# Performance work log

Hardware: AMD Instinct MI355X
Metric: run time of the kernel (lower is better)

## Reference

```python
import jax, jax.numpy as jnp
import numpy as np

D_MODEL = 1024
N_HEADS = 16
D_K = D_MODEL // N_HEADS


def setup_inputs() -> dict:
    key = jax.random.key(0)
    ks = jax.random.split(key, 9)
    s = 0.02
    return {
        "x": jax.random.normal(ks[0], (4, 2048, D_MODEL), dtype=jnp.float32),
        "WQ_w": jax.random.normal(ks[1], (D_MODEL, D_MODEL), dtype=jnp.float32) * s,
        "WQ_b": jax.random.normal(ks[2], (D_MODEL,), dtype=jnp.float32) * s,
        "WK_w": jax.random.normal(ks[3], (D_MODEL, D_MODEL), dtype=jnp.float32) * s,
        "WK_b": jax.random.normal(ks[4], (D_MODEL,), dtype=jnp.float32) * s,
        "WV_w": jax.random.normal(ks[5], (D_MODEL, D_MODEL), dtype=jnp.float32) * s,
        "WV_b": jax.random.normal(ks[6], (D_MODEL,), dtype=jnp.float32) * s,
        "Wo_w": jax.random.normal(ks[7], (D_MODEL, D_MODEL), dtype=jnp.float32) * s,
        "Wo_b": jax.random.normal(ks[8], (D_MODEL,), dtype=jnp.float32) * s,
    }


def _rope_cache(T, dtype):
    half = D_K // 2
    freq = 1.0 / (10000.0 ** (2.0 * jnp.arange(half, dtype=dtype) / D_K))
    angles = jnp.arange(T, dtype=dtype)[:, None] * freq[None, :]  # [T, half]
    return jnp.cos(angles), jnp.sin(angles)


def _apply_rope(x, cos, sin):
    # x: [B, H, T, d_k]; cos/sin: [T, d_k//2] broadcast over B,H
    half = x.shape[-1] // 2
    x1, x2 = x[..., :half], x[..., half:]
    return jnp.concatenate([x1 * cos - x2 * sin, x1 * sin + x2 * cos], axis=-1)


def reference(x, WQ_w, WQ_b, WK_w, WK_b, WV_w, WV_b, Wo_w, Wo_b):
    B, T, D = x.shape

    def proj(w, b):
        y = jnp.einsum('btd,ed->bte', x, w) + b
        return y.reshape(B, T, N_HEADS, D_K).transpose(0, 2, 1, 3)  # [B,H,T,d_k]

    q = proj(WQ_w, WQ_b)
    k = proj(WK_w, WK_b)
    v = proj(WV_w, WV_b)

    cos, sin = _rope_cache(T, x.dtype)
    q = _apply_rope(q, cos, sin)
    k = _apply_rope(k, cos, sin)

    scores = jnp.einsum('bhqd,bhkd->bhqk', q, k) / jnp.sqrt(jnp.asarray(D_K, x.dtype))
    causal = jnp.tril(jnp.ones((T, T), dtype=bool))
    scores = jnp.where(causal[None, None, :, :], scores, -jnp.inf)
    attn = jax.nn.softmax(scores, axis=-1)
    out = jnp.einsum('bhqk,bhkd->bhqd', attn, v)
    out = out.transpose(0, 2, 1, 3).reshape(B, T, D)
    return jnp.einsum('btd,ed->bte', out, Wo_w) + Wo_b
```

## Files before the change

kernel.cpp:

```cpp
#include <hip/hip_runtime.h>
#include <math.h>

#define DM 1024
#define NH 16
#define DK 64
#define BB 4
#define TT 2048
#define MTOT (BB*TT)

typedef __bf16 bf16x8 __attribute__((ext_vector_type(8)));
typedef short  s16x4  __attribute__((ext_vector_type(4)));
typedef float  f32x4  __attribute__((ext_vector_type(4)));

__device__ __forceinline__ short f2bf_s(float f) {
    __bf16 h = (__bf16)f;
    return __builtin_bit_cast(short, h);
}

__device__ __forceinline__ float exp2_fast(float x) {
    float r;
    asm("v_exp_f32 %0, %1" : "=v"(r) : "v"(x));
    return r;
}

__device__ __forceinline__ void async_copy16(unsigned short* lds, const unsigned short* g) {
    __builtin_amdgcn_global_load_lds(
        (const __attribute__((address_space(1))) unsigned int*)g,
        (__attribute__((address_space(3))) unsigned int*)lds, 16, 0, 0);
}

__global__ __launch_bounds__(256)
void cvt_all_kernel(const float* __restrict__ x,
                    const float* __restrict__ wq, const float* __restrict__ wk,
                    const float* __restrict__ wv, const float* __restrict__ wo,
                    unsigned short* __restrict__ xb,
                    unsigned short* __restrict__ wqb, unsigned short* __restrict__ wkb,
                    unsigned short* __restrict__ wvb, unsigned short* __restrict__ wob)
{
    const int XB = (MTOT * DM) / 1024;
    int bz = blockIdx.x;
    const float* src; unsigned short* dst; int blk;
    if (bz < XB) { src = x; dst = xb; blk = bz; }
    else {
        int t = bz - XB, which = t >> 10;
        blk = t & 1023;
        if (which == 0)      { src = wq; dst = wqb; }
        else if (which == 1) { src = wk; dst = wkb; }
        else if (which == 2) { src = wv; dst = wvb; }
        else                 { src = wo; dst = wob; }
    }
    int i = blk * 256 + threadIdx.x;
    float4 v = ((const float4*)src)[i];
    ushort4 o;
    o.x = (unsigned short)f2bf_s(v.x); o.y = (unsigned short)f2bf_s(v.y);
    o.z = (unsigned short)f2bf_s(v.z); o.w = (unsigned short)f2bf_s(v.w);
    ((ushort4*)dst)[i] = o;
}

template<int MODE>
__global__ __launch_bounds__(256, 3)
void gemm_bf16_kernel(const unsigned short* __restrict__ X,
                      const unsigned short* __restrict__ W0, const float* __restrict__ b0,
                      const unsigned short* __restrict__ W1, const float* __restrict__ b1,
                      const unsigned short* __restrict__ W2, const float* __restrict__ b2,
                      void* __restrict__ Y0, void* __restrict__ Y1, void* __restrict__ Y2)
{
    const unsigned short* W; const float* bias; void* Yv;
    const int z = blockIdx.z;
    if (z == 0)      { W = W0; bias = b0; Yv = Y0; }
    else if (z == 1) { W = W1; bias = b1; Yv = Y1; }
    else             { W = W2; bias = b2; Yv = Y2; }

    __shared__ __align__(16) unsigned short As[128 * 64];
    __shared__ __align__(16) unsigned short Bs[128 * 64];

    const int tid  = threadIdx.x;
    const int w    = tid >> 6, lane = tid & 63;
    const int quad = lane >> 4, lq = lane & 15;
    const int bm = blockIdx.x * 128, bn = blockIdx.y * 128;
    const int wm = (w >> 1) * 64,   wn = (w & 1) * 64;

    const int srow = lane >> 3;
    const int sg   = (lane & 7) ^ srow;
    const int soff = sg * 8;

    f32x4 acc[4][4];
    #pragma unroll
    for (int i = 0; i < 4; ++i)
        #pragma unroll
        for (int j = 0; j < 4; ++j)
            acc[i][j] = {0.f, 0.f, 0.f, 0.f};

    for (int k0 = 0; k0 < DM; k0 += 64) {
        #pragma unroll
        for (int c = 0; c < 4; ++c) {
            int r0 = w * 32 + c * 8;
            async_copy16(&As[r0 * 64], &X[(size_t)(bm + r0 + srow) * DM + k0 + soff]);
            async_copy16(&Bs[r0 * 64], &W[(size_t)(bn + r0 + srow) * DM + k0 + soff]);
        }
        __syncthreads();

        #pragma unroll
        for (int ks = 0; ks < 2; ++ks) {
            const int gsw = ((ks << 2) + quad) ^ (lq & 7);
            bf16x8 af[4], bfr[4];
            #pragma unroll
            for (int i = 0; i < 4; ++i)
                af[i] = *(const bf16x8*)&As[(wm + i*16 + lq) * 64 + gsw * 8];
            #pragma unroll
            for (int j = 0; j < 4; ++j)
                bfr[j] = *(const bf16x8*)&Bs[(wn + j*16 + lq) * 64 + gsw * 8];
            #pragma unroll
            for (int i = 0; i < 4; ++i)
                #pragma unroll
                for (int j = 0; j < 4; ++j)
                    acc[i][j] = __builtin_amdgcn_mfma_f32_16x16x32_bf16(af[i], bfr[j], acc[i][j], 0, 0, 0);
        }
        __syncthreads();
    }

    if (MODE == 0) {
        #pragma unroll
        for (int j = 0; j < 4; ++j) {
            int n = bn + wn + j*16 + lq;
            float bv = bias[n];
            #pragma unroll
            for (int i = 0; i < 4; ++i)
                #pragma unroll
                for (int r = 0; r < 4; ++r) {
                    int m = bm + wm + i*16 + quad*4 + r;
                    ((float*)Yv)[(size_t)m * DM + n] = acc[i][j][r] + bv;
                }
        }
    } else if (z == 2) {
        #pragma unroll
        for (int j = 0; j < 4; ++j) {
            int n = bn + wn + j*16 + lq;
            float bv = bias[n];
            int h = n >> 6, dk = n & 63;
            #pragma unroll
            for (int i = 0; i < 4; ++i) {
                int m0 = bm + wm + i*16 + quad*4;
                int b = m0 >> 11, t0 = m0 & 2047;
                ushort4 o;
                o.x = (unsigned short)f2bf_s(acc[i][j][0] + bv);
                o.y = (unsigned short)f2bf_s(acc[i][j][1] + bv);
                o.z = (unsigned short)f2bf_s(acc[i][j][2] + bv);
                o.w = (unsigned short)f2bf_s(acc[i][j][3] + bv);
                *(ushort4*)&((unsigned short*)Yv)[((size_t)(b * NH + h) * DK + dk) * TT + t0] = o;
            }
        }
    } else {
        const float QSC = (z == 0) ? 0.125f * 1.44269504f : 1.0f;
        const int h = (bn + wn) >> 6;
        const int b = (bm + wm) >> 11;
        const int tb0 = ((bm + wm) & 2047) + quad * 4;
        #pragma unroll
        for (int jp = 0; jp < 2; ++jp) {
            int dk1 = jp * 16 + lq;
            float freq = exp2f(-(float)dk1 * 0.4152410118f);
            float bv1 = bias[bn + wn + dk1];
            float bv2 = bias[bn + wn + dk1 + 32];
            float s1, c1, s16v, c16v, sb, cb;
            __sincosf(freq, &s1, &c1);
            __sincosf(16.0f * freq, &s16v, &c16v);
            __sincosf((float)tb0 * freq, &sb, &cb);
            #pragma unroll
            for (int i = 0; i < 4; ++i) {
                float cr = cb, sr = sb;
                #pragma unroll
                for (int r = 0; r < 4; ++r) {
                    int t = tb0 + i*16 + r;
                    float v1 = acc[i][jp][r]     + bv1;
                    float v2 = acc[i][jp + 2][r] + bv2;
                    float o1 = (v1 * cr - v2 * sr) * QSC;
                    float o2 = (v1 * sr + v2 * cr) * QSC;
                    size_t base = ((size_t)(b * NH + h) * TT + t) << 6;
                    ((__bf16*)Yv)[base + dk1]      = (__bf16)o1;
                    ((__bf16*)Yv)[base + dk1 + 32] = (__bf16)o2;
                    float cn = cr * c1 - sr * s1;
                    sr = cr * s1 + sr * c1;
                    cr = cn;
                }
                float cbn = cb * c16v - sb * s16v;
                sb = cb * s16v + sb * c16v;
                cb = cbn;
            }
        }
    }
}

__global__ __launch_bounds__(256, 3)
void attn_kernel(const unsigned short* __restrict__ Q, const unsigned short* __restrict__ K,
                 const unsigned short* __restrict__ Vt_g, unsigned short* __restrict__ ctx)
{
    __shared__ __align__(16) unsigned short KV[2][2][64 * 64];

    const int tid  = threadIdx.x;
    const int w    = tid >> 6, lane = tid & 63;
    const int quad = lane >> 4, lq = lane & 15;
    const int bh = blockIdx.x;
    const int s  = blockIdx.y;
    const int tmap[16] = {15,12,13,14, 8,11,10,9, 7,4,5,6, 0,3,2,1};
    const int t_lo = tmap[s];
    const int qt[2] = { t_lo, t_lo + 16 };
    const size_t kbase = (size_t)bh * TT * DK;
    const size_t vbase = (size_t)bh * DK * TT;

    const int srow = lane >> 3;
    const int sg   = (lane & 7) ^ srow;
    const unsigned short* Ksrc = &K[kbase + (size_t)(w*16 + srow) * DK + sg*8];
    const unsigned short* Vsrc = &Vt_g[vbase + (size_t)(w*16 + srow) * TT + sg*8];

    auto issue = [&](int kb, int buf) {
        unsigned short* Kd = &KV[buf][0][w*16*64];
        unsigned short* Vd = &KV[buf][1][w*16*64];
        const unsigned short* ks0 = Ksrc + (size_t)kb * 64 * DK;
        const unsigned short* vs0 = Vsrc + (size_t)kb * 64;
        async_copy16(Kd,          ks0);
        async_copy16(Kd + 8*64,   ks0 + 8*DK);
        async_copy16(Vd,          vs0);
        async_copy16(Vd + 8*64,   vs0 + (size_t)8*TT);
    };

    int   qrow[2];
    bf16x8 qf[2][2];
    #pragma unroll
    for (int i = 0; i < 2; ++i) {
        qrow[i] = qt[i]*64 + w*16 + lq;
        qf[i][0] = *(const bf16x8*)&Q[kbase + (size_t)qrow[i] * DK + quad*8];
        qf[i][1] = *(const bf16x8*)&Q[kbase + (size_t)qrow[i] * DK + 32 + quad*8];
    }

    f32x4 accO[2][4];
    f32x4 lacc[2] = {{0.f,0.f,0.f,0.f},{0.f,0.f,0.f,0.f}};
    #pragma unroll
    for (int i = 0; i < 2; ++i)
        #pragma unroll
        for (int dt = 0; dt < 4; ++dt) accO[i][dt] = {0.f,0.f,0.f,0.f};

    const int kbmax = qt[1];
    issue(0, 0);
    for (int kb = 0; kb <= kbmax; ++kb) {
        __syncthreads();
        if (kb < kbmax) issue(kb + 1, (kb + 1) & 1);

        const unsigned short* Kb_ = &KV[kb & 1][0][0];
        const unsigned short* Vb_ = &KV[kb & 1][1][0];

        bf16x8 kf[2][4];
        #pragma unroll
        for (int ks = 0; ks < 2; ++ks)
            #pragma unroll
            for (int nt = 0; nt < 4; ++nt)
                kf[ks][nt] = *(const bf16x8*)&Kb_[(nt*16 + lq) * 64 +
                                (((ks << 2) + quad) ^ (lq & 7)) * 8];

        s16x4 p[2][4];
        #pragma unroll
        for (int i = 0; i < 2; ++i) {
            if (kb <= qt[i]) {
                f32x4 st[4];
                #pragma unroll
                for (int nt = 0; nt < 4; ++nt) st[nt] = {0.f,0.f,0.f,0.f};
                __builtin_amdgcn_s_setprio(1);
                #pragma unroll
                for (int ks = 0; ks < 2; ++ks)
                    #pragma unroll
                    for (int nt = 0; nt < 4; ++nt)
                        st[nt] = __builtin_amdgcn_mfma_f32_16x16x32_bf16(kf[ks][nt], qf[i][ks], st[nt], 0, 0, 0);
                __builtin_amdgcn_s_setprio(0);
                if (kb == qt[i]) {
                    #pragma unroll
                    for (int nt = 0; nt < 4; ++nt)
                        #pragma unroll
                        for (int r = 0; r < 4; ++r) {
                            int kc = kb*64 + nt*16 + quad*4 + r;
                            if (kc > qrow[i]) st[nt][r] = -1e30f;
                        }
                }
                #pragma unroll
                for (int nt = 0; nt < 4; ++nt)
                    #pragma unroll
                    for (int r = 0; r < 4; ++r) {
                        float e = exp2_fast(st[nt][r]);
                        lacc[i][r] += e;
                        p[i][nt][r] = f2bf_s(e);
                    }
            }
        }

        #pragma unroll
        for (int ktp = 0; ktp < 2; ++ktp) {
            s16x4 vbh[2][4];
            #pragma unroll
            for (int k2 = 0; k2 < 2; ++k2) {
                int kt = ktp*2 + k2;
                #pragma unroll
                for (int dt = 0; dt < 4; ++dt)
                    vbh[k2][dt] = *(const s16x4*)&Vb_[(dt*16 + lq) * 64 +
                                    (((kt << 1) + (quad >> 1)) ^ (lq & 7)) * 8 +
                                    (quad & 1) * 4];
            }
            __builtin_amdgcn_s_setprio(1);
            #pragma unroll
            for (int i = 0; i < 2; ++i) {
                if (kb <= qt[i]) {
                    #pragma unroll
                    for (int k2 = 0; k2 < 2; ++k2)
                        #pragma unroll
                        for (int dt = 0; dt < 4; ++dt)
                            accO[i][dt] = __builtin_amdgcn_mfma_f32_16x16x16bf16_1k(
                                p[i][ktp*2 + k2], vbh[k2][dt], accO[i][dt], 0, 0, 0);
                }
            }
            __builtin_amdgcn_s_setprio(0);
        }
    }

    const int b = bh >> 4, h = bh & 15;
    #pragma unroll
    for (int i = 0; i < 2; ++i) {
        float l = (lacc[i][0] + lacc[i][1]) + (lacc[i][2] + lacc[i][3]);
        l += __shfl_xor(l, 16, 64);
        l += __shfl_xor(l, 32, 64);
        float linv = 1.0f / l;
        f32x4 il4;
        #pragma unroll
        for (int r = 0; r < 4; ++r) il4[r] = __shfl(linv, quad*4 + r, 64);
        #pragma unroll
        for (int r = 0; r < 4; ++r) {
            int t = qt[i]*64 + w*16 + quad*4 + r;
            size_t ob = ((size_t)b * TT + t) * DM + h * DK;
            #pragma unroll
            for (int dt = 0; dt < 4; ++dt)
                ((__bf16*)ctx)[ob + dt*16 + lq] = (__bf16)(accO[i][dt][r] * il4[r]);
        }
    }
}

extern "C" void kernel_launch(void* const* d_in, const int* in_sizes, int n_in,
                              void* d_out, int out_size, void* d_ws, size_t ws_size,
                              hipStream_t stream)
{
    const float* x   = (const float*)d_in[0];
    const float* WQw = (const float*)d_in[1];
    const float* WQb = (const float*)d_in[2];
    const float* WKw = (const float*)d_in[3];
    const float* WKb = (const float*)d_in[4];
    const float* WVw = (const float*)d_in[5];
    const float* WVb = (const float*)d_in[6];
    const float* WOw = (const float*)d_in[7];
    const float* WOb = (const float*)d_in[8];
    float* out = (float*)d_out;

    unsigned short* ws  = (unsigned short*)d_ws;
    unsigned short* xb  = ws;
    unsigned short* wqb = xb  + (size_t)MTOT * DM;
    unsigned short* wkb = wqb + (size_t)DM * DM;
    unsigned short* wvb = wkb + (size_t)DM * DM;
    unsigned short* wob = wvb + (size_t)DM * DM;
    unsigned short* Qb  = wob + (size_t)DM * DM;
    unsigned short* Kb  = Qb  + (size_t)MTOT * DM;
    unsigned short* Vb  = Kb  + (size_t)MTOT * DM;
    unsigned short* Vtb = Vb  + (size_t)MTOT * DM;
    unsigned short* ctxb = Vb;

    cvt_all_kernel<<<(MTOT*DM)/1024 + 4*(DM*DM)/1024, 256, 0, stream>>>(
        x, WQw, WKw, WVw, WOw, xb, wqb, wkb, wvb, wob);

    gemm_bf16_kernel<1><<<dim3(MTOT/128, DM/128, 3), 256, 0, stream>>>(
        xb, wqb, WQb, wkb, WKb, wvb, WVb, Qb, Kb, Vtb);

    attn_kernel<<<dim3(BB*NH, 16), 256, 0, stream>>>(Qb, Kb, Vtb, ctxb);

    gemm_bf16_kernel<0><<<dim3(MTOT/128, DM/128, 1), 256, 0, stream>>>(
        ctxb, wob, WOb, wob, WOb, wob, WOb, out, out, out);
}
```

Measured before the change: 231.3 us.

## Process one query tile per attention block with longest-first launch order

The attention kernel now handles a single 64-row query tile per block instead of a paired (t, t+16) tile set. The grid doubles to 32 tiles per head and is ordered longest-first, and launch bounds rise to allow 4 blocks per CU. This trades the K/V reuse of the paired tiles for more parallelism, better occupancy and lower register use. Each K/V block is now loaded from global memory by more blocks overall.

Result: slower. 242.3 us (+4.8%).

```diff
diff --git a/kernel.cpp b/kernel.cpp
--- a/kernel.cpp
+++ b/kernel.cpp
@@ -190,7 +190,7 @@
     }
 }
 
-__global__ __launch_bounds__(256, 3)
+__global__ __launch_bounds__(256, 4)
 void attn_kernel(const unsigned short* __restrict__ Q, const unsigned short* __restrict__ K,
                  const unsigned short* __restrict__ Vt_g, unsigned short* __restrict__ ctx)
 {
@@ -200,10 +200,7 @@
     const int w    = tid >> 6, lane = tid & 63;
     const int quad = lane >> 4, lq = lane & 15;
     const int bh = blockIdx.x;
-    const int s  = blockIdx.y;
-    const int tmap[16] = {15,12,13,14, 8,11,10,9, 7,4,5,6, 0,3,2,1};
-    const int t_lo = tmap[s];
-    const int qt[2] = { t_lo, t_lo + 16 };
+    const int qt = 31 - blockIdx.y;
     const size_t kbase = (size_t)bh * TT * DK;
     const size_t vbase = (size_t)bh * DK * TT;
 
@@ -223,72 +220,58 @@
         async_copy16(Vd + 8*64,   vs0 + (size_t)8*TT);
     };
 
-    int   qrow[2];
-    bf16x8 qf[2][2];
+    const int qrow = qt*64 + w*16 + lq;
+    bf16x8 qf[2];
+    qf[0] = *(const bf16x8*)&Q[kbase + (size_t)qrow * DK + quad*8];
+    qf[1] = *(const bf16x8*)&Q[kbase + (size_t)qrow * DK + 32 + quad*8];
+
+    f32x4 accO[4];
+    float l_i = 0.f;
     #pragma unroll
-    for (int i = 0; i < 2; ++i) {
-        qrow[i] = qt[i]*64 + w*16 + lq;
-        qf[i][0] = *(const bf16x8*)&Q[kbase + (size_t)qrow[i] * DK + quad*8];
-        qf[i][1] = *(const bf16x8*)&Q[kbase + (size_t)qrow[i] * DK + 32 + quad*8];
-    }
-
-    f32x4 accO[2][4];
-    f32x4 lacc[2] = {{0.f,0.f,0.f,0.f},{0.f,0.f,0.f,0.f}};
-    #pragma unroll
-    for (int i = 0; i < 2; ++i)
-        #pragma unroll
-        for (int dt = 0; dt < 4; ++dt) accO[i][dt] = {0.f,0.f,0.f,0.f};
-
-    const int kbmax = qt[1];
+    for (int dt = 0; dt < 4; ++dt) accO[dt] = {0.f,0.f,0.f,0.f};
+
     issue(0, 0);
-    for (int kb = 0; kb <= kbmax; ++kb) {
+    for (int kb = 0; kb <= qt; ++kb) {
         __syncthreads();
-        if (kb < kbmax) issue(kb + 1, (kb + 1) & 1);
+        if (kb < qt) issue(kb + 1, (kb + 1) & 1);
 
         const unsigned short* Kb_ = &KV[kb & 1][0][0];
         const unsigned short* Vb_ = &KV[kb & 1][1][0];
 
-        bf16x8 kf[2][4];
-        #pragma unroll
-        for (int ks = 0; ks < 2; ++ks)
+        f32x4 st[4];
+        #pragma unroll
+        for (int nt = 0; nt < 4; ++nt) st[nt] = {0.f,0.f,0.f,0.f};
+        #pragma unroll
+        for (int ks = 0; ks < 2; ++ks) {
+            bf16x8 kfh[4];
             #pragma unroll
             for (int nt = 0; nt < 4; ++nt)
-                kf[ks][nt] = *(const bf16x8*)&Kb_[(nt*16 + lq) * 64 +
+                kfh[nt] = *(const bf16x8*)&Kb_[(nt*16 + lq) * 64 +
                                 (((ks << 2) + quad) ^ (lq & 7)) * 8];
-
-        s16x4 p[2][4];
-        #pragma unroll
-        for (int i = 0; i < 2; ++i) {
-            if (kb <= qt[i]) {
-                f32x4 st[4];
-                #pragma unroll
-                for (int nt = 0; nt < 4; ++nt) st[nt] = {0.f,0.f,0.f,0.f};
-                __builtin_amdgcn_s_setprio(1);
-                #pragma unroll
-                for (int ks = 0; ks < 2; ++ks)
-                    #pragma unroll
-                    for (int nt = 0; nt < 4; ++nt)
-                        st[nt] = __builtin_amdgcn_mfma_f32_16x16x32_bf16(kf[ks][nt], qf[i][ks], st[nt], 0, 0, 0);
-                __builtin_amdgcn_s_setprio(0);
-                if (kb == qt[i]) {
-                    #pragma unroll
-                    for (int nt = 0; nt < 4; ++nt)
-                        #pragma unroll
-                        for (int r = 0; r < 4; ++r) {
-                            int kc = kb*64 + nt*16 + quad*4 + r;
-                            if (kc > qrow[i]) st[nt][r] = -1e30f;
-                        }
+            __builtin_amdgcn_s_setprio(1);
+            #pragma unroll
+            for (int nt = 0; nt < 4; ++nt)
+                st[nt] = __builtin_amdgcn_mfma_f32_16x16x32_bf16(kfh[nt], qf[ks], st[nt], 0, 0, 0);
+            __builtin_amdgcn_s_setprio(0);
+        }
+        if (kb == qt) {
+            #pragma unroll
+            for (int nt = 0; nt < 4; ++nt)
+                #pragma unroll
+                for (int r = 0; r < 4; ++r) {
+                    int kc = kb*64 + nt*16 + quad*4 + r;
+                    if (kc > qrow) st[nt][r] = -1e30f;
                 }
-                #pragma unroll
-                for (int nt = 0; nt < 4; ++nt)
-                    #pragma unroll
-                    for (int r = 0; r < 4; ++r) {
-                        float e = exp2_fast(st[nt][r]);
-                        lacc[i][r] += e;
-                        p[i][nt][r] = f2bf_s(e);
-                    }
+        }
+        s16x4 p[4];
+        #pragma unroll
+        for (int nt = 0; nt < 4; ++nt)
+            #pragma unroll
+            for (int r = 0; r < 4; ++r) {
+                float e = exp2_fast(st[nt][r]);
+                l_i += e;
+                p[nt][r] = f2bf_s(e);
             }
-        }
 
         #pragma unroll
         for (int ktp = 0; ktp < 2; ++ktp) {
@@ -304,38 +287,30 @@
             }
             __builtin_amdgcn_s_setprio(1);
             #pragma unroll
-            for (int i = 0; i < 2; ++i) {
-                if (kb <= qt[i]) {
-                    #pragma unroll
-                    for (int k2 = 0; k2 < 2; ++k2)
-                        #pragma unroll
-                        for (int dt = 0; dt < 4; ++dt)
-                            accO[i][dt] = __builtin_amdgcn_mfma_f32_16x16x16bf16_1k(
-                                p[i][ktp*2 + k2], vbh[k2][dt], accO[i][dt], 0, 0, 0);
-                }
-            }
+            for (int k2 = 0; k2 < 2; ++k2)
+                #pragma unroll
+                for (int dt = 0; dt < 4; ++dt)
+                    accO[dt] = __builtin_amdgcn_mfma_f32_16x16x16bf16_1k(
+                        p[ktp*2 + k2], vbh[k2][dt], accO[dt], 0, 0, 0);
             __builtin_amdgcn_s_setprio(0);
         }
     }
 
     const int b = bh >> 4, h = bh & 15;
+    float l = l_i;
+    l += __shfl_xor(l, 16, 64);
+    l += __shfl_xor(l, 32, 64);
+    float linv = 1.0f / l;
+    f32x4 il4;
     #pragma unroll
-    for (int i = 0; i < 2; ++i) {
-        float l = (lacc[i][0] + lacc[i][1]) + (lacc[i][2] + lacc[i][3]);
-        l += __shfl_xor(l, 16, 64);
-        l += __shfl_xor(l, 32, 64);
-        float linv = 1.0f / l;
-        f32x4 il4;
-        #pragma unroll
-        for (int r = 0; r < 4; ++r) il4[r] = __shfl(linv, quad*4 + r, 64);
-        #pragma unroll
-        for (int r = 0; r < 4; ++r) {
-            int t = qt[i]*64 + w*16 + quad*4 + r;
-            size_t ob = ((size_t)b * TT + t) * DM + h * DK;
-            #pragma unroll
-            for (int dt = 0; dt < 4; ++dt)
-                ((__bf16*)ctx)[ob + dt*16 + lq] = (__bf16)(accO[i][dt][r] * il4[r]);
-        }
+    for (int r = 0; r < 4; ++r) il4[r] = __shfl(linv, quad*4 + r, 64);
+    #pragma unroll
+    for (int r = 0; r < 4; ++r) {
+        int t = qt*64 + w*16 + quad*4 + r;
+        size_t ob = ((size_t)b * TT + t) * DM + h * DK;
+        #pragma unroll
+        for (int dt = 0; dt < 4; ++dt)
+            ((__bf16*)ctx)[ob + dt*16 + lq] = (__bf16)(accO[dt][r] * il4[r]);
     }
 }
 
@@ -372,7 +347,7 @@
     gemm_bf16_kernel<1><<<dim3(MTOT/128, DM/128, 3), 256, 0, stream>>>(
         xb, wqb, WQb, wkb, WKb, wvb, WVb, Qb, Kb, Vtb);
 
-    attn_kernel<<<dim3(BB*NH, 16), 256, 0, stream>>>(Qb, Kb, Vtb, ctxb);
+    attn_kernel<<<dim3(BB*NH, 32), 256, 0, stream>>>(Qb, Kb, Vtb, ctxb);
 
     gemm_bf16_kernel<0><<<dim3(MTOT/128, DM/128, 1), 256, 0, stream>>>(
         ctxb, wob, WOb, wob, WOb, wob, WOb, out, out, out);
```
